# Kernel optimization log

Measured on AMD Instinct MI355X. Metric: run time of the kernel, lower is better.

## Reference

```python
import jax, jax.numpy as jnp
import numpy as np

N_NODES = 100000
N_EDGES = 3200000
N_FEAT = 128
N_HID = 64


def gcn_conv(x, src, dst, ew, W, b, n):
    # x: [N, Fin]; src/dst: [E'] incl. self-loops; ew: [E'] edge weights
    xw = x @ W  # [N, Fout]
    deg = jax.ops.segment_sum(ew, dst, num_segments=n)  # [N]
    dinv = jnp.where(deg > 0, jax.lax.rsqrt(jnp.maximum(deg, 1e-12)), 0.0)
    norm = dinv[src] * ew * dinv[dst]  # [E']
    out = jax.ops.segment_sum(norm[:, None] * xw[src], dst, num_segments=n)
    return out + b


def setup_inputs() -> dict:
    key = jax.random.key(0)
    k = jax.random.split(key, 8)
    x = jax.random.normal(k[0], (N_NODES, N_FEAT), dtype=jnp.float32)
    edge_index = jax.random.randint(k[1], (2, N_EDGES), 0, N_NODES, dtype=jnp.int32)
    edge_attr = jax.random.uniform(k[2], (N_EDGES,), dtype=jnp.float32)
    s1 = 1.0 / np.sqrt(N_FEAT)
    s2 = 1.0 / np.sqrt(N_HID)
    W1 = jax.random.uniform(k[3], (N_FEAT, N_HID), minval=-s1, maxval=s1, dtype=jnp.float32)
    b1 = jnp.zeros((N_HID,), dtype=jnp.float32)
    W2 = jax.random.uniform(k[4], (N_HID, 1), minval=-s2, maxval=s2, dtype=jnp.float32)
    b2 = jnp.zeros((1,), dtype=jnp.float32)
    return {"x": x, "edge_index": edge_index, "edge_attr": edge_attr,
            "W1": W1, "b1": b1, "W2": W2, "b2": b2}


def reference(x, edge_index, edge_attr, W1, b1, W2, b2):
    n = x.shape[0]
    # add self-loops with weight 1 (PyG gcn_norm, improved=False)
    loop = jnp.arange(n, dtype=edge_index.dtype)
    src = jnp.concatenate([edge_index[0], loop])
    dst = jnp.concatenate([edge_index[1], loop])
    ew = jnp.concatenate([edge_attr, jnp.ones((n,), dtype=edge_attr.dtype)])
    h = gcn_conv(x, src, dst, ew, W1, b1, n)
    h = jax.nn.relu(h)
    # dropout is identity in eval mode
    out = gcn_conv(h, src, dst, ew, W2, b2, n)
    return out
```

## Files before the change

### kernel.cpp

```cpp
#include <hip/hip_runtime.h>
#include <hip/hip_fp16.h>


#define NPB_LOG 9
#define NPB     512
#define PCAP    17408

typedef _Float16 f16x8 __attribute__((ext_vector_type(8)));
typedef float    f32x4 __attribute__((ext_vector_type(4)));

__global__ void k_initcur(int* __restrict__ gcur, int npart) {
    int i = blockIdx.x * blockDim.x + threadIdx.x;
    if (i < npart) gcur[i] = i * PCAP;
}

__global__ __launch_bounds__(256) void k_binA(const int* __restrict__ src,
                                              const int* __restrict__ dst,
                                              const float* __restrict__ ea,
                                              int* __restrict__ gcur,
                                              uint2* __restrict__ part,
                                              int E, int npart) {
    __shared__ int hist[256];
    __shared__ int base[256];
    const int ITER = 8;
    int c0 = blockIdx.x * (blockDim.x * ITER);
    hist[threadIdx.x] = 0;
    __syncthreads();
    int dv[ITER];
#pragma unroll
    for (int j = 0; j < ITER; ++j) {
        int e = c0 + j * blockDim.x + threadIdx.x;
        dv[j] = (e < E) ? dst[e] : -1;
        if (dv[j] >= 0) atomicAdd(&hist[dv[j] >> NPB_LOG], 1);
    }
    __syncthreads();
    if (threadIdx.x < npart) {
        int h = hist[threadIdx.x];
        if (h > 0) base[threadIdx.x] = atomicAdd(&gcur[threadIdx.x], h);
    }
    hist[threadIdx.x] = 0;
    __syncthreads();
#pragma unroll
    for (int j = 0; j < ITER; ++j) {
        if (dv[j] >= 0) {
            int e = c0 + j * blockDim.x + threadIdx.x;
            int b = dv[j] >> NPB_LOG;
            int p = base[b] + atomicAdd(&hist[b], 1);
            if (p < (b + 1) * PCAP) {
                uint s = (uint)src[e] | ((uint)(dv[j] & (NPB - 1)) << 17);
                part[p] = make_uint2(s, __float_as_uint(ea[e]));
            }
        }
    }
}

__global__ __launch_bounds__(512) void k_binB(const int* __restrict__ gcur,
                                              const uint2* __restrict__ part,
                                              int2* __restrict__ ecsr,
                                              int* __restrict__ rowstart,
                                              int* __restrict__ cntg,
                                              float* __restrict__ dinv, int n) {
    __shared__ int   cnt[NPB];
    __shared__ float wsum[NPB];
    __shared__ int   cur[NPB];
    __shared__ int   wsums[8];
    int b = blockIdx.x;
    int t = threadIdx.x;
    int lane = t & 63, wv = t >> 6;
    cnt[t] = 0; wsum[t] = 0.0f;
    __syncthreads();
    int beg = b * PCAP;
    int len = gcur[b] - beg;
    if (len > PCAP) len = PCAP;
    for (int j = t; j < len; j += NPB) {
        uint2 ed = part[beg + j];
        int dlow = (ed.x >> 17) & (NPB - 1);
        atomicAdd(&cnt[dlow], 1);
        atomicAdd(&wsum[dlow], __uint_as_float(ed.y));
    }
    __syncthreads();
    int v = cnt[t];
    int s = v;
    for (int off = 1; off < 64; off <<= 1) {
        int u = __shfl_up(s, off, 64);
        if (lane >= off) s += u;
    }
    if (lane == 63) wsums[wv] = s;
    __syncthreads();
    if (t < 64) {
        int x = (t < 8) ? wsums[t] : 0;
        for (int off = 1; off < 8; off <<= 1) {
            int u = __shfl_up(x, off, 64);
            if (lane >= off) x += u;
        }
        if (t < 8) wsums[t] = x;
    }
    __syncthreads();
    int excl = s - v + (wv > 0 ? wsums[wv - 1] : 0);
    cur[t] = excl;
    int node = (b << NPB_LOG) + t;
    if (node < n) {
        rowstart[node] = beg + excl;
        cntg[node]     = v;
        dinv[node]     = rsqrtf(1.0f + wsum[t]);
    }
    __syncthreads();
    for (int j = t; j < len; j += NPB) {
        uint2 ed = part[beg + j];
        int dlow = (ed.x >> 17) & (NPB - 1);
        int p = atomicAdd(&cur[dlow], 1);
        ecsr[beg + p] = make_int2((int)(ed.x & 0x1FFFF), (int)ed.y);
    }
}

#define XPAD 136
__global__ __launch_bounds__(256) void k_gemm1m(const float* __restrict__ x,
                                                const float* __restrict__ W1,
                                                const float* __restrict__ dinv,
                                                __half* __restrict__ xw2, int n) {
    __shared__ __align__(16) _Float16 xs[64 * XPAD];
    __shared__ __align__(16) _Float16 wt[64 * XPAD];
    int tid = threadIdx.x;
    int row0 = blockIdx.x * 64;
    for (int i = tid; i < 64 * 32; i += 256) {
        int r = i >> 5, k4 = i & 31;
        float4 f = make_float4(0.f, 0.f, 0.f, 0.f);
        int gr = row0 + r;
        if (gr < n) f = ((const float4*)x)[(size_t)gr * 32 + k4];
        union { _Float16 h[4]; uint2 u; } tmp;
        tmp.h[0] = (_Float16)f.x; tmp.h[1] = (_Float16)f.y;
        tmp.h[2] = (_Float16)f.z; tmp.h[3] = (_Float16)f.w;
        *(uint2*)&xs[r * XPAD + k4 * 4] = tmp.u;
    }
    for (int i = tid; i < 128 * 64; i += 256) {
        int k = i >> 6, nn = i & 63;
        wt[nn * XPAD + k] = (_Float16)W1[i];
    }
    __syncthreads();

    int strip = tid >> 6;
    int lane  = tid & 63;
    int quad  = lane >> 4;
    int m     = lane & 15;
    f32x4 acc[4] = {{0,0,0,0},{0,0,0,0},{0,0,0,0},{0,0,0,0}};
#pragma unroll
    for (int kc = 0; kc < 4; ++kc) {
        f16x8 a = *(const f16x8*)&xs[(strip * 16 + m) * XPAD + kc * 32 + quad * 8];
#pragma unroll
        for (int nt = 0; nt < 4; ++nt) {
            f16x8 b = *(const f16x8*)&wt[(nt * 16 + m) * XPAD + kc * 32 + quad * 8];
            acc[nt] = __builtin_amdgcn_mfma_f32_16x16x32_f16(a, b, acc[nt], 0, 0, 0);
        }
    }
    float dv[4];
#pragma unroll
    for (int reg = 0; reg < 4; ++reg) {
        int gr = row0 + strip * 16 + quad * 4 + reg;
        dv[reg] = (gr < n) ? dinv[gr] : 0.0f;
    }
#pragma unroll
    for (int nt = 0; nt < 4; ++nt) {
#pragma unroll
        for (int reg = 0; reg < 4; ++reg) {
            int gr = row0 + strip * 16 + quad * 4 + reg;
            if (gr < n)
                xw2[(size_t)gr * 64 + nt * 16 + m] = __float2half(dv[reg] * acc[nt][reg]);
        }
    }
}

__global__ __launch_bounds__(256) void k_agg1f(const int* __restrict__ rowstart,
                                               const int* __restrict__ cntg,
                                               const int2* __restrict__ ecsr,
                                               const float* __restrict__ dinv,
                                               const __half* __restrict__ xw2,
                                               const float* __restrict__ b1,
                                               const float* __restrict__ W2,
                                               float* __restrict__ g, int n) {
    int i = blockIdx.x * 4 + (threadIdx.x >> 6);
    int lane = threadIdx.x & 63;
    if (i >= n) return;
    size_t beg = (size_t)rowstart[i];
    int len = cntg[i];
    float acc = __half2float(xw2[(size_t)i * 64 + lane]);
    for (int j0 = 0; j0 < len; j0 += 64) {
        int idx = j0 + lane;
        int c = 0; float w = 0.0f;
        if (idx < len) {
            int2 ed = ecsr[beg + idx];
            c = ed.x;
            w = __int_as_float(ed.y);
        }
        int m = min(64, len - j0);
        int j = 0;
        for (; j + 4 <= m; j += 4) {
            int   c0 = __shfl(c, j,     64);
            int   c1 = __shfl(c, j + 1, 64);
            int   c2 = __shfl(c, j + 2, 64);
            int   c3 = __shfl(c, j + 3, 64);
            float w0 = __shfl(w, j,     64);
            float w1 = __shfl(w, j + 1, 64);
            float w2 = __shfl(w, j + 2, 64);
            float w3 = __shfl(w, j + 3, 64);
            float v0 = __half2float(xw2[(size_t)c0 * 64 + lane]);
            float v1 = __half2float(xw2[(size_t)c1 * 64 + lane]);
            float v2 = __half2float(xw2[(size_t)c2 * 64 + lane]);
            float v3 = __half2float(xw2[(size_t)c3 * 64 + lane]);
            acc += w0 * v0; acc += w1 * v1; acc += w2 * v2; acc += w3 * v3;
        }
        for (; j < m; ++j) {
            int   cj = __shfl(c, j, 64);
            float wj = __shfl(w, j, 64);
            acc += wj * __half2float(xw2[(size_t)cj * 64 + lane]);
        }
    }
    float di = dinv[i];
    float h = fmaxf(di * acc + b1[lane], 0.0f) * W2[lane];
    for (int off = 32; off; off >>= 1) h += __shfl_down(h, off, 64);
    if (lane == 0) g[i] = di * h;
}

__global__ __launch_bounds__(256) void k_agg2(const int* __restrict__ rowstart,
                                              const int* __restrict__ cntg,
                                              const int2* __restrict__ ecsr,
                                              const float* __restrict__ dinv,
                                              const float* __restrict__ g,
                                              const float* __restrict__ b2,
                                              float* __restrict__ out, int n) {
    int i = blockIdx.x * 4 + (threadIdx.x >> 6);
    int lane = threadIdx.x & 63;
    if (i >= n) return;
    size_t beg = (size_t)rowstart[i];
    int len = cntg[i];
    float p = 0.0f;
    for (int j = lane; j < len; j += 64) {
        int2 ed = ecsr[beg + j];
        p += __int_as_float(ed.y) * g[ed.x];
    }
    for (int off = 32; off; off >>= 1) p += __shfl_down(p, off, 64);
    if (lane == 0) out[i] = b2[0] + dinv[i] * (g[i] + p);
}

extern "C" void kernel_launch(void* const* d_in, const int* in_sizes, int n_in,
                              void* d_out, int out_size, void* d_ws, size_t ws_size,
                              hipStream_t stream) {
    const float* x  = (const float*)d_in[0];
    const int*   ei = (const int*)  d_in[1];
    const float* ea = (const float*)d_in[2];
    const float* W1 = (const float*)d_in[3];
    const float* b1 = (const float*)d_in[4];
    const float* W2 = (const float*)d_in[5];
    const float* b2 = (const float*)d_in[6];
    float* out = (float*)d_out;

    int n = in_sizes[0] / 128;
    int E = in_sizes[1] / 2;
    const int* src = ei;
    const int* dst = ei + E;
    int npart = (n + NPB - 1) >> NPB_LOG;

    int*    ws       = (int*)d_ws;
    int*    gcur     = ws;
    uint2*  part     = (uint2*)(ws + 256);
    __half* xw2      = (__half*)part;
    size_t  psz      = (size_t)npart * PCAP;
    int2*   ecsr     = (int2*)(ws + 256 + psz * 2);
    int*    rowstart = ws + 256 + psz * 4;
    int*    cntg     = rowstart + n;
    float*  dinv     = (float*)(cntg + n);
    float*  g        = dinv + n;

    k_initcur<<<1, 256, 0, stream>>>(gcur, npart);
    k_binA  <<<(E + 2047) / 2048, 256, 0, stream>>>(src, dst, ea, gcur, part, E, npart);
    k_binB  <<<npart, NPB, 0, stream>>>(gcur, part, ecsr, rowstart, cntg, dinv, n);
    k_gemm1m<<<(n + 63) / 64, 256, 0, stream>>>(x, W1, dinv, xw2, n);
    k_agg1f <<<(n + 3) / 4, 256, 0, stream>>>(rowstart, cntg, ecsr, dinv, xw2, b1, W2, g, n);
    k_agg2  <<<(n + 3) / 4, 256, 0, stream>>>(rowstart, cntg, ecsr, dinv, g, b2, out, n);
}
```

Baseline: 367.5 us.

## Stage binned edges in LDS for coalesced partition writes; unroll agg1 gather by 8

k_binA now handles 8192 edges per block. It counts them per partition, prefix-scans the counts, and sorts the edges into an LDS staging buffer ordered by partition, so each partition's edges go to global memory as contiguous runs instead of scattered 8-byte writes. This targets scattered-store cost in the binning pass, at the price of about 74 KB of LDS per block (lower occupancy), fewer blocks, and re-reading dst from global. Separately, the aggregation gather loop in the first layer is unrolled from 4 to 8 edges to keep more loads in flight.

```diff
diff --git a/kernel.cpp b/kernel.cpp
--- a/kernel.cpp
+++ b/kernel.cpp
@@ -5,6 +5,7 @@
 #define NPB_LOG 9
 #define NPB     512
 #define PCAP    17408
+#define NEDG    8192
 
 typedef _Float16 f16x8 __attribute__((ext_vector_type(8)));
 typedef float    f32x4 __attribute__((ext_vector_type(4)));
@@ -20,37 +21,52 @@
                                               int* __restrict__ gcur,
                                               uint2* __restrict__ part,
                                               int E, int npart) {
+    __shared__ uint2 stag[NEDG];
+    __shared__ unsigned char stagb[NEDG];
     __shared__ int hist[256];
+    __shared__ int lofs[256];
     __shared__ int base[256];
-    const int ITER = 8;
-    int c0 = blockIdx.x * (blockDim.x * ITER);
-    hist[threadIdx.x] = 0;
-    __syncthreads();
-    int dv[ITER];
-#pragma unroll
-    for (int j = 0; j < ITER; ++j) {
-        int e = c0 + j * blockDim.x + threadIdx.x;
-        dv[j] = (e < E) ? dst[e] : -1;
-        if (dv[j] >= 0) atomicAdd(&hist[dv[j] >> NPB_LOG], 1);
-    }
-    __syncthreads();
-    if (threadIdx.x < npart) {
-        int h = hist[threadIdx.x];
-        if (h > 0) base[threadIdx.x] = atomicAdd(&gcur[threadIdx.x], h);
-    }
-    hist[threadIdx.x] = 0;
-    __syncthreads();
-#pragma unroll
-    for (int j = 0; j < ITER; ++j) {
-        if (dv[j] >= 0) {
-            int e = c0 + j * blockDim.x + threadIdx.x;
-            int b = dv[j] >> NPB_LOG;
-            int p = base[b] + atomicAdd(&hist[b], 1);
-            if (p < (b + 1) * PCAP) {
-                uint s = (uint)src[e] | ((uint)(dv[j] & (NPB - 1)) << 17);
-                part[p] = make_uint2(s, __float_as_uint(ea[e]));
-            }
-        }
+    int t = threadIdx.x;
+    int c0 = blockIdx.x * NEDG;
+    hist[t] = 0;
+    __syncthreads();
+    for (int j = t; j < NEDG; j += 256) {
+        int e = c0 + j;
+        if (e < E) atomicAdd(&hist[dst[e] >> NPB_LOG], 1);
+    }
+    __syncthreads();
+    int v = hist[t];
+    lofs[t] = v;
+    __syncthreads();
+    for (int off = 1; off < 256; off <<= 1) {
+        int u = (t >= off) ? lofs[t - off] : 0;
+        __syncthreads();
+        lofs[t] += u;
+        __syncthreads();
+    }
+    int excl = lofs[t] - v;
+    if (t < npart && v > 0) base[t] = atomicAdd(&gcur[t], v);
+    __syncthreads();
+    lofs[t] = excl;
+    hist[t] = excl;
+    __syncthreads();
+    for (int j = t; j < NEDG; j += 256) {
+        int e = c0 + j;
+        if (e < E) {
+            int d = dst[e];
+            int b = d >> NPB_LOG;
+            int p = atomicAdd(&hist[b], 1);
+            stag[p]  = make_uint2((uint)src[e] | ((uint)(d & (NPB - 1)) << 17),
+                                  __float_as_uint(ea[e]));
+            stagb[p] = (unsigned char)b;
+        }
+    }
+    __syncthreads();
+    int nvalid = min(NEDG, E - c0);
+    for (int j = t; j < nvalid; j += 256) {
+        int b = stagb[j];
+        int gp = base[b] + (j - lofs[b]);
+        if (gp < (b + 1) * PCAP) part[gp] = stag[j];
     }
 }
 
@@ -193,20 +209,33 @@
         }
         int m = min(64, len - j0);
         int j = 0;
-        for (; j + 4 <= m; j += 4) {
+        for (; j + 8 <= m; j += 8) {
             int   c0 = __shfl(c, j,     64);
             int   c1 = __shfl(c, j + 1, 64);
             int   c2 = __shfl(c, j + 2, 64);
             int   c3 = __shfl(c, j + 3, 64);
+            int   c4 = __shfl(c, j + 4, 64);
+            int   c5 = __shfl(c, j + 5, 64);
+            int   c6 = __shfl(c, j + 6, 64);
+            int   c7 = __shfl(c, j + 7, 64);
             float w0 = __shfl(w, j,     64);
             float w1 = __shfl(w, j + 1, 64);
             float w2 = __shfl(w, j + 2, 64);
             float w3 = __shfl(w, j + 3, 64);
+            float w4 = __shfl(w, j + 4, 64);
+            float w5 = __shfl(w, j + 5, 64);
+            float w6 = __shfl(w, j + 6, 64);
+            float w7 = __shfl(w, j + 7, 64);
             float v0 = __half2float(xw2[(size_t)c0 * 64 + lane]);
             float v1 = __half2float(xw2[(size_t)c1 * 64 + lane]);
             float v2 = __half2float(xw2[(size_t)c2 * 64 + lane]);
             float v3 = __half2float(xw2[(size_t)c3 * 64 + lane]);
+            float v4 = __half2float(xw2[(size_t)c4 * 64 + lane]);
+            float v5 = __half2float(xw2[(size_t)c5 * 64 + lane]);
+            float v6 = __half2float(xw2[(size_t)c6 * 64 + lane]);
+            float v7 = __half2float(xw2[(size_t)c7 * 64 + lane]);
             acc += w0 * v0; acc += w1 * v1; acc += w2 * v2; acc += w3 * v3;
+            acc += w4 * v4; acc += w5 * v5; acc += w6 * v6; acc += w7 * v7;
         }
         for (; j < m; ++j) {
             int   cj = __shfl(c, j, 64);
@@ -271,7 +300,7 @@
     float*  g        = dinv + n;
 
     k_initcur<<<1, 256, 0, stream>>>(gcur, npart);
-    k_binA  <<<(E + 2047) / 2048, 256, 0, stream>>>(src, dst, ea, gcur, part, E, npart);
+    k_binA  <<<(E + NEDG - 1) / NEDG, 256, 0, stream>>>(src, dst, ea, gcur, part, E, npart);
     k_binB  <<<npart, NPB, 0, stream>>>(gcur, part, ecsr, rowstart, cntg, dinv, n);
     k_gemm1m<<<(n + 63) / 64, 256, 0, stream>>>(x, W1, dinv, xw2, n);
     k_agg1f <<<(n + 3) / 4, 256, 0, stream>>>(rowstart, cntg, ecsr, dinv, xw2, b1, W2, g, n);
```

Result: faster. 341.8 us (-7.0%).

## Use finer 64-node partitions for edge binning and unroll aggregation by eight

Applied to the files above, without the earlier changes.

The edge partitioning changes from 512-node buckets (about 196 partitions) to 64-node buckets (about 1563 partitions). The first binning pass now uses larger per-block edge chunks and a shared histogram sized to all partitions. The second binning pass uses 256 threads and a single-wave scan, so many more blocks run in parallel with smaller per-block work. The layer-1 aggregation loop is also unrolled to eight gathers per step to keep more loads in flight. In exchange, the global atomics on partition cursors grow with the number of partitions, and the per-partition capacity margin of 2432 slots for about 2112 expected edges may overflow on skewed inputs.

```diff
diff --git a/kernel.cpp b/kernel.cpp
--- a/kernel.cpp
+++ b/kernel.cpp
@@ -2,9 +2,11 @@
 #include <hip/hip_fp16.h>
 
 
-#define NPB_LOG 9
-#define NPB     512
-#define PCAP    17408
+#define NPB_LOG 6
+#define NPB     64
+#define PCAP    2432
+#define MAXPART 1600
+#define NEDG    8192
 
 typedef _Float16 f16x8 __attribute__((ext_vector_type(8)));
 typedef float    f32x4 __attribute__((ext_vector_type(4)));
@@ -20,41 +22,41 @@
                                               int* __restrict__ gcur,
                                               uint2* __restrict__ part,
                                               int E, int npart) {
-    __shared__ int hist[256];
-    __shared__ int base[256];
-    const int ITER = 8;
-    int c0 = blockIdx.x * (blockDim.x * ITER);
-    hist[threadIdx.x] = 0;
-    __syncthreads();
+    __shared__ int hist[MAXPART];
+    __shared__ int base[MAXPART];
+    int t = threadIdx.x;
+    int c0 = blockIdx.x * NEDG;
+    for (int i = t; i < npart; i += 256) hist[i] = 0;
+    __syncthreads();
+    const int ITER = NEDG / 256;
     int dv[ITER];
 #pragma unroll
     for (int j = 0; j < ITER; ++j) {
-        int e = c0 + j * blockDim.x + threadIdx.x;
+        int e = c0 + j * 256 + t;
         dv[j] = (e < E) ? dst[e] : -1;
         if (dv[j] >= 0) atomicAdd(&hist[dv[j] >> NPB_LOG], 1);
     }
     __syncthreads();
-    if (threadIdx.x < npart) {
-        int h = hist[threadIdx.x];
-        if (h > 0) base[threadIdx.x] = atomicAdd(&gcur[threadIdx.x], h);
-    }
-    hist[threadIdx.x] = 0;
+    for (int i = t; i < npart; i += 256) {
+        int h = hist[i];
+        if (h > 0) base[i] = atomicAdd(&gcur[i], h);
+        hist[i] = 0;
+    }
     __syncthreads();
 #pragma unroll
     for (int j = 0; j < ITER; ++j) {
         if (dv[j] >= 0) {
-            int e = c0 + j * blockDim.x + threadIdx.x;
+            int e = c0 + j * 256 + t;
             int b = dv[j] >> NPB_LOG;
             int p = base[b] + atomicAdd(&hist[b], 1);
-            if (p < (b + 1) * PCAP) {
-                uint s = (uint)src[e] | ((uint)(dv[j] & (NPB - 1)) << 17);
-                part[p] = make_uint2(s, __float_as_uint(ea[e]));
-            }
-        }
-    }
-}
-
-__global__ __launch_bounds__(512) void k_binB(const int* __restrict__ gcur,
+            if (p < (b + 1) * PCAP)
+                part[p] = make_uint2((uint)src[e] | ((uint)(dv[j] & (NPB - 1)) << 17),
+                                     __float_as_uint(ea[e]));
+        }
+    }
+}
+
+__global__ __launch_bounds__(256) void k_binB(const int* __restrict__ gcur,
                                               const uint2* __restrict__ part,
                                               int2* __restrict__ ecsr,
                                               int* __restrict__ rowstart,
@@ -63,49 +65,37 @@
     __shared__ int   cnt[NPB];
     __shared__ float wsum[NPB];
     __shared__ int   cur[NPB];
-    __shared__ int   wsums[8];
-    int b = blockIdx.x;
-    int t = threadIdx.x;
-    int lane = t & 63, wv = t >> 6;
-    cnt[t] = 0; wsum[t] = 0.0f;
+    int b = blockIdx.x, t = threadIdx.x;
+    if (t < NPB) { cnt[t] = 0; wsum[t] = 0.0f; }
     __syncthreads();
     int beg = b * PCAP;
     int len = gcur[b] - beg;
     if (len > PCAP) len = PCAP;
-    for (int j = t; j < len; j += NPB) {
+    for (int j = t; j < len; j += 256) {
         uint2 ed = part[beg + j];
         int dlow = (ed.x >> 17) & (NPB - 1);
         atomicAdd(&cnt[dlow], 1);
         atomicAdd(&wsum[dlow], __uint_as_float(ed.y));
     }
     __syncthreads();
-    int v = cnt[t];
-    int s = v;
-    for (int off = 1; off < 64; off <<= 1) {
-        int u = __shfl_up(s, off, 64);
-        if (lane >= off) s += u;
-    }
-    if (lane == 63) wsums[wv] = s;
-    __syncthreads();
     if (t < 64) {
-        int x = (t < 8) ? wsums[t] : 0;
-        for (int off = 1; off < 8; off <<= 1) {
-            int u = __shfl_up(x, off, 64);
-            if (lane >= off) x += u;
-        }
-        if (t < 8) wsums[t] = x;
-    }
-    __syncthreads();
-    int excl = s - v + (wv > 0 ? wsums[wv - 1] : 0);
-    cur[t] = excl;
-    int node = (b << NPB_LOG) + t;
-    if (node < n) {
-        rowstart[node] = beg + excl;
-        cntg[node]     = v;
-        dinv[node]     = rsqrtf(1.0f + wsum[t]);
-    }
-    __syncthreads();
-    for (int j = t; j < len; j += NPB) {
+        int v = cnt[t];
+        int s = v;
+        for (int off = 1; off < 64; off <<= 1) {
+            int u = __shfl_up(s, off, 64);
+            if (t >= off) s += u;
+        }
+        int excl = s - v;
+        cur[t] = excl;
+        int node = (b << NPB_LOG) + t;
+        if (node < n) {
+            rowstart[node] = beg + excl;
+            cntg[node]     = v;
+            dinv[node]     = rsqrtf(1.0f + wsum[t]);
+        }
+    }
+    __syncthreads();
+    for (int j = t; j < len; j += 256) {
         uint2 ed = part[beg + j];
         int dlow = (ed.x >> 17) & (NPB - 1);
         int p = atomicAdd(&cur[dlow], 1);
@@ -193,20 +183,33 @@
         }
         int m = min(64, len - j0);
         int j = 0;
-        for (; j + 4 <= m; j += 4) {
+        for (; j + 8 <= m; j += 8) {
             int   c0 = __shfl(c, j,     64);
             int   c1 = __shfl(c, j + 1, 64);
             int   c2 = __shfl(c, j + 2, 64);
             int   c3 = __shfl(c, j + 3, 64);
+            int   c4 = __shfl(c, j + 4, 64);
+            int   c5 = __shfl(c, j + 5, 64);
+            int   c6 = __shfl(c, j + 6, 64);
+            int   c7 = __shfl(c, j + 7, 64);
             float w0 = __shfl(w, j,     64);
             float w1 = __shfl(w, j + 1, 64);
             float w2 = __shfl(w, j + 2, 64);
             float w3 = __shfl(w, j + 3, 64);
+            float w4 = __shfl(w, j + 4, 64);
+            float w5 = __shfl(w, j + 5, 64);
+            float w6 = __shfl(w, j + 6, 64);
+            float w7 = __shfl(w, j + 7, 64);
             float v0 = __half2float(xw2[(size_t)c0 * 64 + lane]);
             float v1 = __half2float(xw2[(size_t)c1 * 64 + lane]);
             float v2 = __half2float(xw2[(size_t)c2 * 64 + lane]);
             float v3 = __half2float(xw2[(size_t)c3 * 64 + lane]);
+            float v4 = __half2float(xw2[(size_t)c4 * 64 + lane]);
+            float v5 = __half2float(xw2[(size_t)c5 * 64 + lane]);
+            float v6 = __half2float(xw2[(size_t)c6 * 64 + lane]);
+            float v7 = __half2float(xw2[(size_t)c7 * 64 + lane]);
             acc += w0 * v0; acc += w1 * v1; acc += w2 * v2; acc += w3 * v3;
+            acc += w4 * v4; acc += w5 * v5; acc += w6 * v6; acc += w7 * v7;
         }
         for (; j < m; ++j) {
             int   cj = __shfl(c, j, 64);
@@ -261,18 +264,18 @@
 
     int*    ws       = (int*)d_ws;
     int*    gcur     = ws;
-    uint2*  part     = (uint2*)(ws + 256);
+    uint2*  part     = (uint2*)(ws + MAXPART);
     __half* xw2      = (__half*)part;
     size_t  psz      = (size_t)npart * PCAP;
-    int2*   ecsr     = (int2*)(ws + 256 + psz * 2);
-    int*    rowstart = ws + 256 + psz * 4;
+    int2*   ecsr     = (int2*)(ws + MAXPART + psz * 2);
+    int*    rowstart = ws + MAXPART + psz * 4;
     int*    cntg     = rowstart + n;
     float*  dinv     = (float*)(cntg + n);
     float*  g        = dinv + n;
 
-    k_initcur<<<1, 256, 0, stream>>>(gcur, npart);
-    k_binA  <<<(E + 2047) / 2048, 256, 0, stream>>>(src, dst, ea, gcur, part, E, npart);
-    k_binB  <<<npart, NPB, 0, stream>>>(gcur, part, ecsr, rowstart, cntg, dinv, n);
+    k_initcur<<<(npart + 255) / 256, 256, 0, stream>>>(gcur, npart);
+    k_binA  <<<(E + NEDG - 1) / NEDG, 256, 0, stream>>>(src, dst, ea, gcur, part, E, npart);
+    k_binB  <<<npart, 256, 0, stream>>>(gcur, part, ecsr, rowstart, cntg, dinv, n);
     k_gemm1m<<<(n + 63) / 64, 256, 0, stream>>>(x, W1, dinv, xw2, n);
     k_agg1f <<<(n + 3) / 4, 256, 0, stream>>>(rowstart, cntg, ecsr, dinv, xw2, b1, W2, g, n);
     k_agg2  <<<(n + 3) / 4, 256, 0, stream>>>(rowstart, cntg, ecsr, dinv, g, b2, out, n);
```

After: 356.0 us. -3.1%, faster.
